# Kernel tuning notes

Measured on AMD Instinct MI355X. Metric: run time of the kernel, lower is better.

The kernel has to match this reference:

```python
import jax, jax.numpy as jnp
import numpy as np

T, B, D, NQ = 1024, 4096, 16, 4  # seq_len, batch, input_dim, n_qubits (= hidden_dim)


def _qlayer(angles, phi):
    """Simulate: RX(angles) encode + trainable RX(phi) per wire + CNOT chain + PauliZ expvals.
    Since the initial state is |0..0> and all single-qubit gates are RX (which compose as
    RX(a)RX(b)=RX(a+b)), the pre-entanglement state is a product state with per-wire
    probabilities p1 = sin^2((a+phi)/2); CNOTs permute basis states, hence permute probs.
    Returns <Z_w> per wire, shape [B, n]."""
    Bsz, n = angles.shape
    theta = angles + phi[None, :]
    p1 = jnp.sin(0.5 * theta) ** 2  # [B, n]
    probs = jnp.ones((Bsz, 1), angles.dtype)
    for w in range(n):  # outer product over wires -> [B, 2^n], wire 0 = most significant
        pw = jnp.stack([1.0 - p1[:, w], p1[:, w]], axis=-1)  # [B, 2]
        probs = (probs[:, :, None] * pw[:, None, :]).reshape(Bsz, -1)
    psi = probs.reshape((Bsz,) + (2,) * n)
    for c in range(n - 1):  # CNOT(c, c+1): flip target amplitudes where control = 1
        ax = c + 1
        s0 = jnp.take(psi, 0, axis=ax)
        s1 = jnp.flip(jnp.take(psi, 1, axis=ax), axis=ax)  # target axis after removal = ax
        psi = jnp.stack([s0, s1], axis=ax)
    probs = psi.reshape(Bsz, -1)
    bits = (jnp.arange(2 ** n)[None, :] >> (n - 1 - jnp.arange(n))[:, None]) & 1  # [n, 2^n]
    signs = (1 - 2 * bits).astype(angles.dtype)
    return probs @ signs.T  # [B, n]


def setup_inputs() -> dict:
    key = jax.random.key(0)
    ks = jax.random.split(key, 16)
    H = NQ  # hidden_dim == n_qubits structurally
    s = 0.1
    inp = {
        "inputs": jax.random.normal(ks[0], (T, B, D), dtype=jnp.float32),
        "W_f": jax.random.normal(ks[1], (NQ, D + H), dtype=jnp.float32) * s,
        "b_f": jax.random.normal(ks[2], (NQ,), dtype=jnp.float32) * s,
        "W_i": jax.random.normal(ks[3], (NQ, D + H), dtype=jnp.float32) * s,
        "b_i": jax.random.normal(ks[4], (NQ,), dtype=jnp.float32) * s,
        "W_g": jax.random.normal(ks[5], (NQ, D + H), dtype=jnp.float32) * s,
        "b_g": jax.random.normal(ks[6], (NQ,), dtype=jnp.float32) * s,
        "W_o": jax.random.normal(ks[7], (NQ, D + H), dtype=jnp.float32) * s,
        "b_o": jax.random.normal(ks[8], (NQ,), dtype=jnp.float32) * s,
        "rx_f": jax.random.normal(ks[9], (NQ,), dtype=jnp.float32),
        "rx_i": jax.random.normal(ks[10], (NQ,), dtype=jnp.float32),
        "rx_g": jax.random.normal(ks[11], (NQ,), dtype=jnp.float32),
        "rx_o": jax.random.normal(ks[12], (NQ,), dtype=jnp.float32),
    }
    return inp


def reference(inputs, W_f, b_f, W_i, b_i, W_g, b_g, W_o, b_o, rx_f, rx_i, rx_g, rx_o):
    Tn, Bn, Dn = inputs.shape
    H = rx_f.shape[0]
    hx = jnp.zeros((Bn, H), inputs.dtype)
    cx = jnp.zeros((Bn, H), inputs.dtype)

    def step(carry, x):
        hx, cx = carry
        comb = jnp.concatenate([x, hx], axis=1)  # [B, D+H]
        f = jax.nn.sigmoid(_qlayer(comb @ W_f.T + b_f, rx_f))
        i = jax.nn.sigmoid(_qlayer(comb @ W_i.T + b_i, rx_i))
        g = jnp.tanh(_qlayer(comb @ W_g.T + b_g, rx_g))
        o = jax.nn.sigmoid(_qlayer(comb @ W_o.T + b_o, rx_o))
        cx2 = f * cx + i * g
        hx2 = o * jnp.tanh(cx2)
        return (hx2, cx2), hx2

    (hx, cx), stacked = jax.lax.scan(step, (hx, cx), inputs)
    return stacked, hx, cx
```

## Files before the change

### kernel.cpp

```cpp
#include <hip/hip_runtime.h>

#define T_LEN 1024
#define B_SZ  4096
#define CHUNK 32
#define NCHUNK (T_LEN / CHUNK)

#define DPP_QP(a,b,c,d) ((a)|((b)<<2)|((c)<<4)|((d)<<6))
#define DPP_QPX1 DPP_QP(1,0,3,2)
#define DPP_QPX2 DPP_QP(2,3,0,1)
#define DPP_QPX3 DPP_QP(3,2,1,0)
#define DPP_BCAST0 DPP_QP(0,0,0,0)
#define DPP_BCAST1 DPP_QP(1,1,1,1)
#define DPP_BCAST2 DPP_QP(2,2,2,2)
#define DPP_BCAST3 DPP_QP(3,3,3,3)
#define DPP_ROW_SHR(n) (0x110|(n))
#define DPP_ROW_ROR(n) (0x120|(n))

template <int CTRL>
__device__ __forceinline__ float dppf(float x) {
  return __int_as_float(__builtin_amdgcn_update_dpp(
      0, __float_as_int(x), CTRL, 0xF, 0xF, true));
}
template <int CTRL>
__device__ __forceinline__ float dppf_id1(float x) {
  return __int_as_float(__builtin_amdgcn_update_dpp(
      0x3f800000, __float_as_int(x), CTRL, 0xF, 0xF, false));
}

__global__ void __launch_bounds__(128, 2) qlstm_65481071402744_kernel(
    const float* __restrict__ x,
    const float* __restrict__ Wf, const float* __restrict__ bfv,
    const float* __restrict__ Wi, const float* __restrict__ biv,
    const float* __restrict__ Wg, const float* __restrict__ bgv,
    const float* __restrict__ Wo, const float* __restrict__ bov,
    const float* __restrict__ rxf, const float* __restrict__ rxi,
    const float* __restrict__ rxg, const float* __restrict__ rxo,
    float* __restrict__ out) {
  __shared__ float zbuf[2][CHUNK][64];

  const int tid = threadIdx.x;
  const int lane = tid & 63;
  const int g = lane & 3;
  const int w = (lane >> 2) & 3;
  const int b = (blockIdx.x << 2) + (lane >> 4);

  auto Wsel = [&](int gg) -> const float* {
    return gg == 0 ? Wf : gg == 1 ? Wi : gg == 2 ? Wg : Wo;
  };
  const float* bown = g == 0 ? bfv : g == 1 ? biv : g == 2 ? bgv : bov;
  const float* rxown = g == 0 ? rxf : g == 1 ? rxi : g == 2 ? rxg : rxo;
  constexpr float INV2PI = 0.15915494309189535f;

  if (tid >= 64) {
    float Wxp[4][4];
#pragma unroll
    for (int j = 0; j < 4; ++j) {
      const float* Wt = Wsel(g ^ j);
#pragma unroll
      for (int d = 0; d < 4; ++d)
        Wxp[j][d] = Wt[w * 20 + (g << 2) + d] * INV2PI;
    }
    const float zinit = (bown[w] + rxown[w]) * INV2PI;

    const float4* xp4 = (const float4*)x + ((size_t)b << 2) + g;
    float4 xr[8];
#pragma unroll
    for (int u = 0; u < 8; ++u) xr[u] = xp4[(size_t)u * (B_SZ * 4)];

    for (int c = 0; c < NCHUNK; ++c) {
      float* zb = &zbuf[c & 1][0][0];
#pragma unroll
      for (int qq = 0; qq < CHUNK / 8; ++qq) {
#pragma unroll
        for (int u = 0; u < 8; ++u) {
          const int tloc = (qq << 3) + u;
          const int t = c * CHUNK + tloc;
          const float4 xq = xr[u];
          int tl = t + 8;
          tl = tl < T_LEN ? tl : T_LEN - 1;
          xr[u] = xp4[(size_t)tl * (B_SZ * 4)];

          float p0 = fmaf(Wxp[0][0], xq.x, zinit);
          p0 = fmaf(Wxp[0][1], xq.y, p0);
          p0 = fmaf(Wxp[0][2], xq.z, p0);
          p0 = fmaf(Wxp[0][3], xq.w, p0);
          float p1 = fmaf(Wxp[1][3], xq.w,
                     fmaf(Wxp[1][2], xq.z,
                     fmaf(Wxp[1][1], xq.y, Wxp[1][0] * xq.x)));
          float p2 = fmaf(Wxp[2][3], xq.w,
                     fmaf(Wxp[2][2], xq.z,
                     fmaf(Wxp[2][1], xq.y, Wxp[2][0] * xq.x)));
          float p3 = fmaf(Wxp[3][3], xq.w,
                     fmaf(Wxp[3][2], xq.z,
                     fmaf(Wxp[3][1], xq.y, Wxp[3][0] * xq.x)));

          const float zx = (p0 + dppf<DPP_QPX1>(p1)) +
                           (dppf<DPP_QPX2>(p2) + dppf<DPP_QPX3>(p3));
          zb[tloc * 64 + lane] = __builtin_amdgcn_fractf(zx);
        }
      }
      __syncthreads();
    }
  } else {
    const float* Wown = Wsel(g);
    float Whs[4];
#pragma unroll
    for (int k = 0; k < 4; ++k)
      Whs[k] = Wown[w * 20 + 16 + ((w + k) & 3)] * INV2PI;

    constexpr float L2E = 1.4426950408889634f;
    const bool isG = (g == 2);
    const float nlscale = isG ? -2.0f * L2E : -L2E;
    const float nla = isG ? 2.0f : 1.0f;
    const float nlb = isG ? -1.0f : 0.0f;

    float hx = 0.0f, cx = 0.0f;
    float* outp = out + ((size_t)b << 2) + w;

    for (int c = 0; c < NCHUNK; ++c) {
      __syncthreads();
      const float* zb = &zbuf[c & 1][0][0];
#pragma unroll
      for (int qq = 0; qq < CHUNK / 8; ++qq) {
        float hb[8];
#pragma unroll
        for (int u = 0; u < 8; ++u) {
          const int tloc = (qq << 3) + u;
          const float zxf = zb[tloc * 64 + lane];

          const float h1 = dppf<DPP_ROW_ROR(12)>(hx);
          const float h2 = dppf<DPP_ROW_ROR(8)>(hx);
          const float h3 = dppf<DPP_ROW_ROR(4)>(hx);
          float za = fmaf(Whs[0], hx, zxf);
          za = fmaf(Whs[1], h1, za);
          const float zb2 = fmaf(Whs[3], h3, Whs[2] * h2);
          const float z = za + zb2;

          const float ccos = __builtin_amdgcn_cosf(z);

          float q = ccos * dppf_id1<DPP_ROW_SHR(4)>(ccos);
          q = q * dppf_id1<DPP_ROW_SHR(8)>(q);

          const float ee = __builtin_amdgcn_exp2f(q * nlscale);
          const float s = fmaf(__builtin_amdgcn_rcpf(1.0f + ee), nla, nlb);

          const float fA = dppf<DPP_BCAST0>(s);
          const float iA = dppf<DPP_BCAST1>(s);
          const float gA = dppf<DPP_BCAST2>(s);
          const float oA = dppf<DPP_BCAST3>(s);

          cx = fmaf(fA, cx, iA * gA);
          const float e3 = __builtin_amdgcn_exp2f(cx * (-2.0f * L2E));
          const float th = fmaf(2.0f, __builtin_amdgcn_rcpf(1.0f + e3), -1.0f);
          hx = oA * th;
          hb[u] = hx;
        }
        if (g == 0) {
          const int tbase = c * CHUNK + (qq << 3);
#pragma unroll
          for (int u = 0; u < 8; ++u)
            outp[(size_t)(tbase + u) * (B_SZ * 4)] = hb[u];
        }
      }
    }

    if (g == 0) {
      const size_t base = (size_t)T_LEN * B_SZ * 4;
      out[base + (b << 2) + w] = hx;
      out[base + B_SZ * 4 + (b << 2) + w] = cx;
    }
  }
}

extern "C" void kernel_launch(void* const* d_in, const int* in_sizes, int n_in,
                              void* d_out, int out_size, void* d_ws, size_t ws_size,
                              hipStream_t stream) {
  const float* x   = (const float*)d_in[0];
  const float* Wf  = (const float*)d_in[1];
  const float* bf_ = (const float*)d_in[2];
  const float* Wi  = (const float*)d_in[3];
  const float* bi_ = (const float*)d_in[4];
  const float* Wg  = (const float*)d_in[5];
  const float* bg_ = (const float*)d_in[6];
  const float* Wo  = (const float*)d_in[7];
  const float* bo_ = (const float*)d_in[8];
  const float* rxf = (const float*)d_in[9];
  const float* rxi = (const float*)d_in[10];
  const float* rxg = (const float*)d_in[11];
  const float* rxo = (const float*)d_in[12];

  qlstm_65481071402744_kernel<<<B_SZ / 4, 128, 0, stream>>>(
      x, Wf, bf_, Wi, bi_, Wg, bg_, Wo, bo_, rxf, rxi, rxg, rxo,
      (float*)d_out);
}
```

Baseline: 430.5 us.

## Interleave four batch groups per consumer wave to hide recurrence latency

Each block now covers 16 batch elements instead of 4. A single consumer wave advances four independent LSTM recurrences in an interleaved loop, and two producer waves each compute input projections for two batch groups. The goal is to fill the dependent DPP/transcendental latency chain with independent work and cut the number of blocks from 1024 to 256. The trade-off is more registers per consumer, fewer waves in total (256 blocks of 3 waves, which may underfill the CUs), and a smaller chunk, which means more barriers.

After: 608.2 us. 1.41x slower.

```diff
diff --git a/kernel.cpp b/kernel.cpp
--- a/kernel.cpp
+++ b/kernel.cpp
@@ -2,8 +2,9 @@
 
 #define T_LEN 1024
 #define B_SZ  4096
-#define CHUNK 32
+#define CHUNK 16
 #define NCHUNK (T_LEN / CHUNK)
+#define NC 4
 
 #define DPP_QP(a,b,c,d) ((a)|((b)<<2)|((c)<<4)|((d)<<6))
 #define DPP_QPX1 DPP_QP(1,0,3,2)
@@ -27,7 +28,7 @@
       0x3f800000, __float_as_int(x), CTRL, 0xF, 0xF, false));
 }
 
-__global__ void __launch_bounds__(128, 2) qlstm_65481071402744_kernel(
+__global__ void __launch_bounds__(192, 1) qlstm_65481071402744_kernel(
     const float* __restrict__ x,
     const float* __restrict__ Wf, const float* __restrict__ bfv,
     const float* __restrict__ Wi, const float* __restrict__ biv,
@@ -36,13 +37,16 @@
     const float* __restrict__ rxf, const float* __restrict__ rxi,
     const float* __restrict__ rxg, const float* __restrict__ rxo,
     float* __restrict__ out) {
-  __shared__ float zbuf[2][CHUNK][64];
+  __shared__ float zbuf[2][CHUNK][64 * NC];
 
   const int tid = threadIdx.x;
+  const int wv = tid >> 6;
   const int lane = tid & 63;
   const int g = lane & 3;
   const int w = (lane >> 2) & 3;
-  const int b = (blockIdx.x << 2) + (lane >> 4);
+  const int bq = lane >> 4;
+  const int b0 = (blockIdx.x << 4) + bq;
+  const bool prod = (wv != 0);
 
   auto Wsel = [&](int gg) -> const float* {
     return gg == 0 ? Wf : gg == 1 ? Wi : gg == 2 ? Wg : Wo;
@@ -50,9 +54,15 @@
   const float* bown = g == 0 ? bfv : g == 1 ? biv : g == 2 ? bgv : bov;
   const float* rxown = g == 0 ? rxf : g == 1 ? rxi : g == 2 ? rxg : rxo;
   constexpr float INV2PI = 0.15915494309189535f;
-
-  if (tid >= 64) {
-    float Wxp[4][4];
+  constexpr float L2E = 1.4426950408889634f;
+
+  float Wxp[4][4];
+  float zinit = 0.0f;
+  const float4 *xpA = nullptr, *xpB = nullptr;
+  float4 xrA[8], xrB[8];
+  int col = 0;
+  if (prod) {
+    const int pw = wv - 1;
 #pragma unroll
     for (int j = 0; j < 4; ++j) {
       const float* Wt = Wsel(g ^ j);
@@ -60,114 +70,132 @@
       for (int d = 0; d < 4; ++d)
         Wxp[j][d] = Wt[w * 20 + (g << 2) + d] * INV2PI;
     }
-    const float zinit = (bown[w] + rxown[w]) * INV2PI;
-
-    const float4* xp4 = (const float4*)x + ((size_t)b << 2) + g;
-    float4 xr[8];
-#pragma unroll
-    for (int u = 0; u < 8; ++u) xr[u] = xp4[(size_t)u * (B_SZ * 4)];
-
-    for (int c = 0; c < NCHUNK; ++c) {
+    zinit = (bown[w] + rxown[w]) * INV2PI;
+    xpA = (const float4*)x + ((size_t)(b0 + 4 * (2 * pw + 0)) << 2) + g;
+    xpB = (const float4*)x + ((size_t)(b0 + 4 * (2 * pw + 1)) << 2) + g;
+#pragma unroll
+    for (int u = 0; u < 8; ++u) {
+      xrA[u] = xpA[(size_t)u * (B_SZ * 4)];
+      xrB[u] = xpB[(size_t)u * (B_SZ * 4)];
+    }
+    col = (pw << 7) + lane;
+  }
+
+  auto xdot = [&](const float4& xq) -> float {
+    float p0 = fmaf(Wxp[0][0], xq.x, zinit);
+    p0 = fmaf(Wxp[0][1], xq.y, p0);
+    p0 = fmaf(Wxp[0][2], xq.z, p0);
+    p0 = fmaf(Wxp[0][3], xq.w, p0);
+    float p1 = fmaf(Wxp[1][3], xq.w,
+               fmaf(Wxp[1][2], xq.z,
+               fmaf(Wxp[1][1], xq.y, Wxp[1][0] * xq.x)));
+    float p2 = fmaf(Wxp[2][3], xq.w,
+               fmaf(Wxp[2][2], xq.z,
+               fmaf(Wxp[2][1], xq.y, Wxp[2][0] * xq.x)));
+    float p3 = fmaf(Wxp[3][3], xq.w,
+               fmaf(Wxp[3][2], xq.z,
+               fmaf(Wxp[3][1], xq.y, Wxp[3][0] * xq.x)));
+    const float zx = (p0 + dppf<DPP_QPX1>(p1)) +
+                     (dppf<DPP_QPX2>(p2) + dppf<DPP_QPX3>(p3));
+    return __builtin_amdgcn_fractf(zx);
+  };
+
+  const float* Wown = Wsel(g);
+  float Whs[4];
+#pragma unroll
+  for (int k = 0; k < 4; ++k)
+    Whs[k] = Wown[w * 20 + 16 + ((w + k) & 3)] * INV2PI;
+  const bool isG = (g == 2);
+  const float nlscale = isG ? -2.0f * L2E : -L2E;
+  const float nla = isG ? 2.0f : 1.0f;
+  const float nlb = isG ? -1.0f : 0.0f;
+  float hx[NC], cx[NC];
+  float* outp[NC];
+#pragma unroll
+  for (int j = 0; j < NC; ++j) {
+    hx[j] = 0.0f;
+    cx[j] = 0.0f;
+    outp[j] = out + ((size_t)(b0 + 4 * j) << 2) + w;
+  }
+
+  for (int c = 0; c < NCHUNK; ++c) {
+    if (prod) {
       float* zb = &zbuf[c & 1][0][0];
 #pragma unroll
+      for (int tloc = 0; tloc < CHUNK; ++tloc) {
+        const int t = c * CHUNK + tloc;
+        int tl = t + 8;
+        tl = tl < T_LEN ? tl : T_LEN - 1;
+        const float4 xqA = xrA[tloc & 7];
+        xrA[tloc & 7] = xpA[(size_t)tl * (B_SZ * 4)];
+        zb[tloc * (64 * NC) + col] = xdot(xqA);
+        const float4 xqB = xrB[tloc & 7];
+        xrB[tloc & 7] = xpB[(size_t)tl * (B_SZ * 4)];
+        zb[tloc * (64 * NC) + col + 64] = xdot(xqB);
+      }
+    }
+
+    __syncthreads();
+
+    if (!prod) {
+      const float* zb = &zbuf[c & 1][0][0];
+#pragma unroll
       for (int qq = 0; qq < CHUNK / 8; ++qq) {
+        float hb[NC][8];
 #pragma unroll
         for (int u = 0; u < 8; ++u) {
           const int tloc = (qq << 3) + u;
-          const int t = c * CHUNK + tloc;
-          const float4 xq = xr[u];
-          int tl = t + 8;
-          tl = tl < T_LEN ? tl : T_LEN - 1;
-          xr[u] = xp4[(size_t)tl * (B_SZ * 4)];
-
-          float p0 = fmaf(Wxp[0][0], xq.x, zinit);
-          p0 = fmaf(Wxp[0][1], xq.y, p0);
-          p0 = fmaf(Wxp[0][2], xq.z, p0);
-          p0 = fmaf(Wxp[0][3], xq.w, p0);
-          float p1 = fmaf(Wxp[1][3], xq.w,
-                     fmaf(Wxp[1][2], xq.z,
-                     fmaf(Wxp[1][1], xq.y, Wxp[1][0] * xq.x)));
-          float p2 = fmaf(Wxp[2][3], xq.w,
-                     fmaf(Wxp[2][2], xq.z,
-                     fmaf(Wxp[2][1], xq.y, Wxp[2][0] * xq.x)));
-          float p3 = fmaf(Wxp[3][3], xq.w,
-                     fmaf(Wxp[3][2], xq.z,
-                     fmaf(Wxp[3][1], xq.y, Wxp[3][0] * xq.x)));
-
-          const float zx = (p0 + dppf<DPP_QPX1>(p1)) +
-                           (dppf<DPP_QPX2>(p2) + dppf<DPP_QPX3>(p3));
-          zb[tloc * 64 + lane] = __builtin_amdgcn_fractf(zx);
-        }
-      }
-      __syncthreads();
-    }
-  } else {
-    const float* Wown = Wsel(g);
-    float Whs[4];
-#pragma unroll
-    for (int k = 0; k < 4; ++k)
-      Whs[k] = Wown[w * 20 + 16 + ((w + k) & 3)] * INV2PI;
-
-    constexpr float L2E = 1.4426950408889634f;
-    const bool isG = (g == 2);
-    const float nlscale = isG ? -2.0f * L2E : -L2E;
-    const float nla = isG ? 2.0f : 1.0f;
-    const float nlb = isG ? -1.0f : 0.0f;
-
-    float hx = 0.0f, cx = 0.0f;
-    float* outp = out + ((size_t)b << 2) + w;
-
-    for (int c = 0; c < NCHUNK; ++c) {
-      __syncthreads();
-      const float* zb = &zbuf[c & 1][0][0];
-#pragma unroll
-      for (int qq = 0; qq < CHUNK / 8; ++qq) {
-        float hb[8];
-#pragma unroll
-        for (int u = 0; u < 8; ++u) {
-          const int tloc = (qq << 3) + u;
-          const float zxf = zb[tloc * 64 + lane];
-
-          const float h1 = dppf<DPP_ROW_ROR(12)>(hx);
-          const float h2 = dppf<DPP_ROW_ROR(8)>(hx);
-          const float h3 = dppf<DPP_ROW_ROR(4)>(hx);
-          float za = fmaf(Whs[0], hx, zxf);
-          za = fmaf(Whs[1], h1, za);
-          const float zb2 = fmaf(Whs[3], h3, Whs[2] * h2);
-          const float z = za + zb2;
-
-          const float ccos = __builtin_amdgcn_cosf(z);
-
-          float q = ccos * dppf_id1<DPP_ROW_SHR(4)>(ccos);
-          q = q * dppf_id1<DPP_ROW_SHR(8)>(q);
-
-          const float ee = __builtin_amdgcn_exp2f(q * nlscale);
-          const float s = fmaf(__builtin_amdgcn_rcpf(1.0f + ee), nla, nlb);
-
-          const float fA = dppf<DPP_BCAST0>(s);
-          const float iA = dppf<DPP_BCAST1>(s);
-          const float gA = dppf<DPP_BCAST2>(s);
-          const float oA = dppf<DPP_BCAST3>(s);
-
-          cx = fmaf(fA, cx, iA * gA);
-          const float e3 = __builtin_amdgcn_exp2f(cx * (-2.0f * L2E));
-          const float th = fmaf(2.0f, __builtin_amdgcn_rcpf(1.0f + e3), -1.0f);
-          hx = oA * th;
-          hb[u] = hx;
+#pragma unroll
+          for (int j = 0; j < NC; ++j) {
+            const float zxf = zb[tloc * (64 * NC) + (j << 6) + lane];
+
+            const float h1 = dppf<DPP_ROW_ROR(12)>(hx[j]);
+            const float h2 = dppf<DPP_ROW_ROR(8)>(hx[j]);
+            const float h3 = dppf<DPP_ROW_ROR(4)>(hx[j]);
+            float za = fmaf(Whs[0], hx[j], zxf);
+            za = fmaf(Whs[1], h1, za);
+            const float zb2 = fmaf(Whs[3], h3, Whs[2] * h2);
+            const float z = za + zb2;
+
+            const float ccos = __builtin_amdgcn_cosf(z);
+
+            float q = ccos * dppf_id1<DPP_ROW_SHR(4)>(ccos);
+            q = q * dppf_id1<DPP_ROW_SHR(8)>(q);
+
+            const float ee = __builtin_amdgcn_exp2f(q * nlscale);
+            const float s = fmaf(__builtin_amdgcn_rcpf(1.0f + ee), nla, nlb);
+
+            const float fA = dppf<DPP_BCAST0>(s);
+            const float iA = dppf<DPP_BCAST1>(s);
+            const float gA = dppf<DPP_BCAST2>(s);
+            const float oA = dppf<DPP_BCAST3>(s);
+
+            cx[j] = fmaf(fA, cx[j], iA * gA);
+            const float e3 = __builtin_amdgcn_exp2f(cx[j] * (-2.0f * L2E));
+            const float th =
+                fmaf(2.0f, __builtin_amdgcn_rcpf(1.0f + e3), -1.0f);
+            hx[j] = oA * th;
+            hb[j][u] = hx[j];
+          }
         }
         if (g == 0) {
           const int tbase = c * CHUNK + (qq << 3);
 #pragma unroll
-          for (int u = 0; u < 8; ++u)
-            outp[(size_t)(tbase + u) * (B_SZ * 4)] = hb[u];
+          for (int j = 0; j < NC; ++j)
+#pragma unroll
+            for (int u = 0; u < 8; ++u)
+              outp[j][(size_t)(tbase + u) * (B_SZ * 4)] = hb[j][u];
         }
       }
     }
-
-    if (g == 0) {
-      const size_t base = (size_t)T_LEN * B_SZ * 4;
-      out[base + (b << 2) + w] = hx;
-      out[base + B_SZ * 4 + (b << 2) + w] = cx;
+  }
+
+  if (!prod && g == 0) {
+    const size_t base = (size_t)T_LEN * B_SZ * 4;
+#pragma unroll
+    for (int j = 0; j < NC; ++j) {
+      out[base + ((b0 + 4 * j) << 2) + w] = hx[j];
+      out[base + B_SZ * 4 + ((b0 + 4 * j) << 2) + w] = cx[j];
     }
   }
 }
@@ -189,7 +217,7 @@
   const float* rxg = (const float*)d_in[11];
   const float* rxo = (const float*)d_in[12];
 
-  qlstm_65481071402744_kernel<<<B_SZ / 4, 128, 0, stream>>>(
+  qlstm_65481071402744_kernel<<<B_SZ / 16, 192, 0, stream>>>(
       x, Wf, bf_, Wi, bi_, Wg, bg_, Wo, bo_, rxf, rxi, rxg, rxo,
       (float*)d_out);
 }
```
